# Kernel optimization log

Hardware: AMD Instinct MI355X
Metric: run time of the kernel (lower is better)

## Reference

```python
import jax, jax.numpy as jnp
import numpy as np

N, S, D, H, E, ETYPES = 1024, 64, 256, 4, 4096, 4
HD = D // H
EPS = 1e-5


def setup_inputs() -> dict:
    key = jax.random.key(0)
    ks = jax.random.split(key, 8)
    node_features = jax.random.normal(ks[0], (N, S, D), dtype=jnp.float32)
    lengths = jax.random.randint(ks[1], (N,), 1, S + 1)
    node_masks = (jnp.arange(S)[None, :] < lengths[:, None]).astype(jnp.float32)
    # unique edges (torch builds an adjacency matrix, so duplicates collapse)
    rng = np.random.default_rng(0)
    cand = rng.integers(0, N, size=(4 * E, 2))
    uniq = np.unique(cand, axis=0)
    assert uniq.shape[0] >= E
    perm = rng.permutation(uniq.shape[0])[:E]
    edge_index = jnp.asarray(uniq[perm].T, dtype=jnp.int64)  # [2, E]
    edge_type = jnp.asarray(rng.integers(1, ETYPES + 1, size=(E,)), dtype=jnp.int64)
    scale = 0.02
    wq = jax.random.normal(ks[2], (D, D), jnp.float32) * scale
    wk = jax.random.normal(ks[3], (D, D), jnp.float32) * scale
    wv = jax.random.normal(ks[4], (D, D), jnp.float32) * scale
    wo = jax.random.normal(ks[5], (D, D), jnp.float32) * scale
    return dict(
        node_features=node_features, node_masks=node_masks,
        ln_w=jnp.ones((D,), jnp.float32), ln_b=jnp.zeros((D,), jnp.float32),
        wq=wq, bq=jnp.zeros((D,), jnp.float32),
        wk=wk, bk=jnp.zeros((D,), jnp.float32),
        wv=wv, bv=jnp.zeros((D,), jnp.float32),
        wo=wo, bo=jnp.zeros((D,), jnp.float32),
        edge_type_weights=jnp.ones((ETYPES,), jnp.float32),
        edge_index=edge_index, edge_type=edge_type,
    )


def reference(node_features, node_masks, ln_w, ln_b, wq, bq, wk, bk, wv, bv,
              wo, bo, edge_type_weights, edge_index, edge_type):
    n, s, d = node_features.shape
    # LayerNorm (biased variance, eps=1e-5, as torch)
    mu = jnp.mean(node_features, axis=-1, keepdims=True)
    var = jnp.mean((node_features - mu) ** 2, axis=-1, keepdims=True)
    xn = (node_features - mu) * jax.lax.rsqrt(var + EPS) * ln_w + ln_b
    q = (xn @ wq + bq).reshape(n, s, H, HD)
    k = (xn @ wk + bk).reshape(n, s, H, HD)
    v = (xn @ wv + bv).reshape(n, s, H, HD)
    src, dst = edge_index[0], edge_index[1]
    # per-edge scalar bias: softplus(edge_type_weights[type-1]).clamp(1e-6, 1e6)
    ew = jnp.clip(jax.nn.softplus(edge_type_weights[edge_type - 1]), 1e-6, 1e6)  # [E]
    qe, ke, ve = q[src], k[dst], v[dst]              # [E,S,H,HD]
    km = node_masks[dst]                              # [E,S] key-side mask
    qm = node_masks[src]                              # [E,S] query-side mask
    scores = jnp.einsum('eqhd,ekhd->ehqk', qe, ke) / jnp.sqrt(jnp.float32(HD))
    scores = scores + ew[:, None, None, None]
    neg = jnp.float32(-1e30)
    scores = jnp.where(km[:, None, None, :] > 0, scores, neg)
    # per-edge softmax over the key node's valid tokens; zero rows where no valid key
    attn = jax.nn.softmax(scores, axis=-1) * km[:, None, None, :]
    ctx = jnp.einsum('ehqk,ekhd->eqhd', attn, ve) * qm[:, :, None, None]  # [E,S,H,HD]
    out = jax.ops.segment_sum(ctx, src, num_segments=n)   # sum over incident edges
    out = out.reshape(n, s, d)
    out = out @ wo + bo                                   # output projection (dropout=eval noop)
    out = out + node_features                             # residual
    return out * node_masks[..., None]
```

## Files before the change

kernel.cpp:

```cpp
#include <hip/hip_runtime.h>

#define DDIM 256
#define NEDGE 4096
#define SLEN 64
#define NNODE 1024
#define ROWS 65536

typedef short s16x8 __attribute__((ext_vector_type(8)));
typedef float f32x4 __attribute__((ext_vector_type(4)));

static __device__ __forceinline__ unsigned short f2bf(float f){
  union { float f; unsigned u; } v; v.f = f;
  unsigned r = v.u + 0x7FFFu + ((v.u >> 16) & 1u);
  return (unsigned short)(r >> 16);
}

static __device__ __forceinline__ void gl2lds16(const unsigned short* g, unsigned short* l){
  __builtin_amdgcn_global_load_lds((const __attribute__((address_space(1))) unsigned int*)g,
                                   (__attribute__((address_space(3))) unsigned int*)l, 16, 0, 0);
}

__global__ __launch_bounds__(256) void setup_kernel(const float* nf, const float* lnw, const float* lnb,
                                                    const float* wq, const float* wk, const float* wv, const float* wo,
                                                    const float* bq, const float* bk, const float* bv,
                                                    const float* masks, const int* eidx,
                                                    unsigned short* xn, unsigned short* Wqkv, unsigned short* Wo_t,
                                                    float* qkvb, int* lenp, int* deg){
  int bid = blockIdx.x, tid = threadIdx.x;
  if (bid < 16384){
    int lane = tid & 63;
    int row = bid*4 + (tid >> 6);
    const float4 x4 = ((const float4*)(nf + (size_t)row*DDIM))[lane];
    float s  = x4.x + x4.y + x4.z + x4.w;
    float sq = x4.x*x4.x + x4.y*x4.y + x4.z*x4.z + x4.w*x4.w;
    for (int off=1; off<64; off<<=1){ s += __shfl_xor(s, off); sq += __shfl_xor(sq, off); }
    float mu  = s  * (1.0f/DDIM);
    float var = sq * (1.0f/DDIM) - mu*mu;
    float rs  = rsqrtf(var + 1e-5f);
    float4 w4 = ((const float4*)lnw)[lane];
    float4 b4 = ((const float4*)lnb)[lane];
    ushort4 o;
    o.x = f2bf((x4.x - mu)*rs*w4.x + b4.x);
    o.y = f2bf((x4.y - mu)*rs*w4.y + b4.y);
    o.z = f2bf((x4.z - mu)*rs*w4.z + b4.z);
    o.w = f2bf((x4.w - mu)*rs*w4.w + b4.w);
    ((ushort4*)(xn + (size_t)row*DDIM))[lane] = o;
  } else if (bid < 17412){
    int idx = (bid - 16384)*256 + tid;
    if (idx < 196608){
      int mat = idx >> 16;
      int rem = idx & 65535;
      int n = rem >> 8, k = rem & 255;
      const float* W = (mat==0)?wq:(mat==1)?wk:wv;
      Wqkv[(size_t)(mat*256 + n)*256 + k] = f2bf(W[k*256 + n]);
    } else if (idx < 262144){
      int rem = idx - 196608;
      int n = rem >> 8, k = rem & 255;
      Wo_t[(size_t)n*256 + k] = f2bf(wo[k*256 + n]);
    } else if (idx < 262912){
      int i = idx - 262144;
      qkvb[i] = (i < 256) ? bq[i] : (i < 512) ? bk[i-256] : bv[i-512];
    }
  } else if (bid < 17668){
    int lane = tid & 63;
    int node = (bid - 17412)*4 + (tid >> 6);
    unsigned long long b = __ballot(masks[node*SLEN + lane] > 0.f);
    if (lane == 0) lenp[node] = __popcll(b);
  } else {
    int e = (bid - 17668)*256 + tid;
    if (e < NEDGE) atomicAdd(&deg[eidx[e]], 1);
  }
}

__global__ void scan_kernel(const int* deg, int* startp, int* order){
  __shared__ int buf[NNODE];
  __shared__ int hist[65];
  int t = threadIdx.x;
  int d = deg[t];
  buf[t] = d;
  if (t < 65) hist[t] = 0;
  __syncthreads();
  for (int off=1; off<NNODE; off<<=1){
    int v = (t >= off) ? buf[t-off] : 0;
    __syncthreads();
    buf[t] += v;
    __syncthreads();
  }
  startp[t] = buf[t] - d;
  int dc = d > 64 ? 64 : d;
  atomicAdd(&hist[dc], 1);
  __syncthreads();
  if (t == 0){
    int acc = 0;
    for (int i = 64; i >= 0; i--){ int h = hist[i]; hist[i] = acc; acc += h; }
  }
  __syncthreads();
  int pos = atomicAdd(&hist[dc], 1);
  order[pos] = t;
}

__global__ __launch_bounds__(256) void edge_fill_kernel(const int* eidx, const int* startp, int* cursor, int* elist){
  int e = blockIdx.x*256 + threadIdx.x;
  if (e < NEDGE){
    int s = eidx[e];
    int p = atomicAdd(&cursor[s], 1);
    elist[startp[s] + p] = eidx[NEDGE + e];
  }
}

__global__ __launch_bounds__(256) void qkv_kernel(const unsigned short* xn, const unsigned short* Wqkv,
                                                  const float* qkvb,
                                                  unsigned short* qb, unsigned short* kb_, unsigned short* vb){
  __shared__ __align__(16) unsigned short As[4096];
  __shared__ __align__(16) unsigned short Bs[8192];
  int tid = threadIdx.x;
  int lane = tid & 63, wid = tid >> 6, m = lane & 15, quad = lane >> 4;
  int row0 = blockIdx.x * 64;
  int col0 = blockIdx.y * 128;
  int rw = (wid & 1) * 32, cw = (wid >> 1) * 64;
  f32x4 acc[8];
  #pragma unroll
  for (int i=0;i<8;i++) acc[i] = (f32x4){0.f,0.f,0.f,0.f};
  for (int kc = 0; kc < 4; kc++){
    __syncthreads();
    #pragma unroll
    for (int i=0;i<2;i++){
      int cid = i*256 + tid, row = cid >> 3, c8 = cid & 7;
      gl2lds16(xn + (size_t)(row0 + row)*DDIM + kc*64 + ((c8 ^ (row&7))<<3), As + cid*8);
    }
    #pragma unroll
    for (int i=0;i<4;i++){
      int cid = i*256 + tid, row = cid >> 3, c8 = cid & 7;
      gl2lds16(Wqkv + (size_t)(col0 + row)*DDIM + kc*64 + ((c8 ^ (row&7))<<3), Bs + cid*8);
    }
    __syncthreads();
    #pragma unroll
    for (int ks=0; ks<2; ks++){
      int sw = ((ks*4 + quad) ^ (m&7)) << 3;
      s16x8 af[2], bf[4];
      #pragma unroll
      for (int mt=0;mt<2;mt++) af[mt] = *(const s16x8*)(As + (rw + mt*16 + m)*64 + sw);
      #pragma unroll
      for (int nt=0;nt<4;nt++) bf[nt] = *(const s16x8*)(Bs + (cw + nt*16 + m)*64 + sw);
      #pragma unroll
      for (int mt=0;mt<2;mt++)
        #pragma unroll
        for (int nt=0;nt<4;nt++)
          acc[mt*4+nt] = __builtin_amdgcn_mfma_f32_16x16x32_bf16(af[mt], bf[nt], acc[mt*4+nt], 0,0,0);
    }
  }
  #pragma unroll
  for (int nt=0;nt<4;nt++){
    int cg = col0 + cw + nt*16 + m;
    int mat = cg >> 8, col = cg & 255;
    unsigned short* ob = (mat==0)?qb:(mat==1)?kb_:vb;
    float bb = qkvb[cg];
    #pragma unroll
    for (int mt=0;mt<2;mt++)
      #pragma unroll
      for (int r=0;r<4;r++){
        int row = row0 + rw + mt*16 + quad*4 + r;
        ob[(size_t)row*DDIM + col] = f2bf(acc[mt*4+nt][r] + bb);
      }
  }
}

__global__ __launch_bounds__(256) void attn_kernel(const unsigned short* qb, const unsigned short* kbuf,
                                                   const unsigned short* vb, const int* lenp,
                                                   const int* startp, const int* degp, const int* elist,
                                                   const int* order, unsigned short* ctxb){
  __shared__ __align__(16) unsigned short Kt[2][4096];
  __shared__ unsigned short Vt[2][4096];
  __shared__ unsigned short P[4096];
  int tid = threadIdx.x;
  int lane = tid & 63, wid = tid >> 6, m = lane & 15, quad = lane >> 4;
  int src = order[blockIdx.x], h = blockIdx.y;
  int ls = lenp[src];
  int qtm = (ls + 15) >> 4;
  int s0 = startp[src], dg = degp[src];
  bool active = wid < qtm;
  unsigned short* Pw = P + wid*1024;

  s16x8 qf0 = {0,0,0,0,0,0,0,0}, qf1 = {0,0,0,0,0,0,0,0};
  if (active){
    const unsigned short* qbase = qb + (size_t)(src*SLEN + wid*16 + m)*DDIM + h*64 + quad*8;
    qf0 = *(const s16x8*)(qbase);
    qf1 = *(const s16x8*)(qbase + 32);
  }
  f32x4 o[4];
  #pragma unroll
  for (int i=0;i<4;i++) o[i] = (f32x4){0.f,0.f,0.f,0.f};

  int dstc = 0, ldc = 0;
  if (dg > 0){
    dstc = elist[s0]; ldc = lenp[dstc];
    #pragma unroll
    for (int i=0;i<2;i++){
      int cid = i*256 + tid, row = cid >> 3, c8 = cid & 7;
      gl2lds16(kbuf + (size_t)(dstc*SLEN + row)*DDIM + h*64 + ((c8 ^ (row&7))<<3), Kt[0] + cid*8);
    }
    const unsigned short* vrow = vb + (size_t)(dstc*SLEN + lane)*DDIM + h*64 + wid*16;
    s16x8 v0 = *(const s16x8*)(vrow);
    s16x8 v1 = *(const s16x8*)(vrow + 8);
    #pragma unroll
    for (int j=0;j<8;j++){
      int d = wid*16 + j;
      Vt[0][d*64 + (((lane>>3)^(d&7))<<3) + (lane&7)] = (unsigned short)v0[j];
    }
    #pragma unroll
    for (int j=0;j<8;j++){
      int d = wid*16 + 8 + j;
      Vt[0][d*64 + (((lane>>3)^(d&7))<<3) + (lane&7)] = (unsigned short)v1[j];
    }
  }
  __syncthreads();

  for (int ei=0; ei<dg; ei++){
    int cur = ei & 1, nxt = cur ^ 1;
    bool have_next = (ei+1 < dg);
    int dstn = 0, ldn = 0;
    s16x8 v0n = {0,0,0,0,0,0,0,0}, v1n = {0,0,0,0,0,0,0,0};
    if (have_next){
      dstn = elist[s0 + ei + 1]; ldn = lenp[dstn];
      #pragma unroll
      for (int i=0;i<2;i++){
        int cid = i*256 + tid, row = cid >> 3, c8 = cid & 7;
        gl2lds16(kbuf + (size_t)(dstn*SLEN + row)*DDIM + h*64 + ((c8 ^ (row&7))<<3), Kt[nxt] + cid*8);
      }
      const unsigned short* vrow = vb + (size_t)(dstn*SLEN + lane)*DDIM + h*64 + wid*16;
      v0n = *(const s16x8*)(vrow);
      v1n = *(const s16x8*)(vrow + 8);
    }
    int ktm = (ldc + 15) >> 4;
    int ks2 = (ktm + 1) >> 1;
    if (active){
      f32x4 acc[4];
      #pragma unroll
      for (int i=0;i<4;i++) acc[i] = (f32x4){0.f,0.f,0.f,0.f};
      #pragma unroll
      for (int kt=0; kt<4; kt++) if (kt < ktm){
        int key = kt*16 + m;
        s16x8 b0 = *(const s16x8*)(Kt[cur] + key*64 + ((quad ^ (m&7))<<3));
        acc[kt] = __builtin_amdgcn_mfma_f32_16x16x32_bf16(qf0, b0, acc[kt], 0,0,0);
        s16x8 b1 = *(const s16x8*)(Kt[cur] + key*64 + (((4 + quad) ^ (m&7))<<3));
        acc[kt] = __builtin_amdgcn_mfma_f32_16x16x32_bf16(qf1, b1, acc[kt], 0,0,0);
      }
      #pragma unroll
      for (int r=0; r<4; r++){
        float x[4];
        #pragma unroll
        for (int kt=0; kt<4; kt++)
          x[kt] = (kt < ktm && kt*16 + m < ldc) ? __expf(acc[kt][r]*0.125f) : 0.f;
        float s = x[0] + x[1] + x[2] + x[3];
        for (int off=1; off<16; off<<=1) s += __shfl_xor(s, off);
        float inv = 1.0f / s;
        int q = quad*4 + r;
        #pragma unroll
        for (int kt=0; kt<4; kt++) if (kt < 2*ks2){
          int key = kt*16 + m;
          Pw[q*64 + (((key>>3)^(q&7))<<3) + (key&7)] = f2bf(x[kt]*inv);
        }
      }
      #pragma unroll
      for (int ks=0; ks<2; ks++) if (ks < ks2){
        s16x8 pa = *(const s16x8*)(Pw + m*64 + ((((ks*4+quad))^(m&7))<<3));
        #pragma unroll
        for (int dt=0; dt<4; dt++){
          int d = dt*16 + m;
          s16x8 vf = *(const s16x8*)(Vt[cur] + d*64 + (((ks*4+quad)^(d&7))<<3));
          o[dt] = __builtin_amdgcn_mfma_f32_16x16x32_bf16(pa, vf, o[dt], 0,0,0);
        }
      }
    }
    if (have_next){
      #pragma unroll
      for (int j=0;j<8;j++){
        int d = wid*16 + j;
        Vt[nxt][d*64 + (((lane>>3)^(d&7))<<3) + (lane&7)] = (unsigned short)v0n[j];
      }
      #pragma unroll
      for (int j=0;j<8;j++){
        int d = wid*16 + 8 + j;
        Vt[nxt][d*64 + (((lane>>3)^(d&7))<<3) + (lane&7)] = (unsigned short)v1n[j];
      }
      dstc = dstn; ldc = ldn;
    }
    __syncthreads();
  }
  if (active){
    #pragma unroll
    for (int dt=0; dt<4; dt++){
      int col = h*64 + dt*16 + m;
      #pragma unroll
      for (int r=0; r<4; r++){
        int row = src*SLEN + wid*16 + quad*4 + r;
        ctxb[(size_t)row*DDIM + col] = f2bf(o[dt][r]);
      }
    }
  }
}

__global__ __launch_bounds__(256) void out_kernel(const unsigned short* ctxb, const unsigned short* Wo_t,
                                                  const float* bo, const float* nf, const float* masks,
                                                  float* out){
  __shared__ __align__(16) unsigned short As[4096];
  __shared__ __align__(16) unsigned short Bs[8192];
  int tid = threadIdx.x;
  int lane = tid & 63, wid = tid >> 6, m = lane & 15, quad = lane >> 4;
  int row0 = blockIdx.x * 64;
  int col0 = blockIdx.y * 128;
  int rw = (wid & 1) * 32, cw = (wid >> 1) * 64;
  f32x4 acc[8];
  #pragma unroll
  for (int i=0;i<8;i++) acc[i] = (f32x4){0.f,0.f,0.f,0.f};
  for (int kc = 0; kc < 4; kc++){
    __syncthreads();
    #pragma unroll
    for (int i=0;i<2;i++){
      int cid = i*256 + tid, row = cid >> 3, c8 = cid & 7;
      gl2lds16(ctxb + (size_t)(row0 + row)*DDIM + kc*64 + ((c8 ^ (row&7))<<3), As + cid*8);
    }
    #pragma unroll
    for (int i=0;i<4;i++){
      int cid = i*256 + tid, row = cid >> 3, c8 = cid & 7;
      gl2lds16(Wo_t + (size_t)(col0 + row)*DDIM + kc*64 + ((c8 ^ (row&7))<<3), Bs + cid*8);
    }
    __syncthreads();
    #pragma unroll
    for (int ks=0; ks<2; ks++){
      int sw = ((ks*4 + quad) ^ (m&7)) << 3;
      s16x8 af[2], bf[4];
      #pragma unroll
      for (int mt=0;mt<2;mt++) af[mt] = *(const s16x8*)(As + (rw + mt*16 + m)*64 + sw);
      #pragma unroll
      for (int nt=0;nt<4;nt++) bf[nt] = *(const s16x8*)(Bs + (cw + nt*16 + m)*64 + sw);
      #pragma unroll
      for (int mt=0;mt<2;mt++)
        #pragma unroll
        for (int nt=0;nt<4;nt++)
          acc[mt*4+nt] = __builtin_amdgcn_mfma_f32_16x16x32_bf16(af[mt], bf[nt], acc[mt*4+nt], 0,0,0);
    }
  }
  #pragma unroll
  for (int nt=0;nt<4;nt++){
    int col = col0 + cw + nt*16 + m;
    float bb = bo[col];
    #pragma unroll
    for (int mt=0;mt<2;mt++)
      #pragma unroll
      for (int r=0;r<4;r++){
        int row = row0 + rw + mt*16 + quad*4 + r;
        float v = acc[mt*4+nt][r] + bb + nf[(size_t)row*DDIM + col];
        out[(size_t)row*DDIM + col] = v * masks[row];
      }
  }
}

extern "C" void kernel_launch(void* const* d_in, const int* in_sizes, int n_in,
                              void* d_out, int out_size, void* d_ws, size_t ws_size,
                              hipStream_t stream){
  const float* nf    = (const float*)d_in[0];
  const float* masks = (const float*)d_in[1];
  const float* lnw   = (const float*)d_in[2];
  const float* lnb   = (const float*)d_in[3];
  const float* wq    = (const float*)d_in[4];
  const float* bq    = (const float*)d_in[5];
  const float* wk    = (const float*)d_in[6];
  const float* bk    = (const float*)d_in[7];
  const float* wv    = (const float*)d_in[8];
  const float* bv    = (const float*)d_in[9];
  const float* wo    = (const float*)d_in[10];
  const float* bo    = (const float*)d_in[11];
  const int*   eidx  = (const int*)d_in[13];
  float* out = (float*)d_out;

  char* ws = (char*)d_ws;
  const size_t B = (size_t)ROWS * DDIM * 2;
  unsigned short* xn   = (unsigned short*)(ws);
  unsigned short* qb   = (unsigned short*)(ws + B);
  unsigned short* kb   = (unsigned short*)(ws + 2*B);
  unsigned short* vb   = (unsigned short*)(ws + 3*B);
  unsigned short* ctxb = (unsigned short*)(ws + 4*B);
  char* wp = ws + 5*B;
  unsigned short* Wqkv = (unsigned short*)(wp);
  unsigned short* Wo_t = (unsigned short*)(wp + 393216);
  float* qkvb         = (float*)(wp + 524288);
  char* ip = wp + 528384;
  int* deg    = (int*)(ip);
  int* cursor = (int*)(ip + 4096);
  int* startp = (int*)(ip + 8192);
  int* lenp   = (int*)(ip + 12288);
  int* order  = (int*)(ip + 16384);
  int* elist  = (int*)(ip + 20480);

  hipMemsetAsync(deg, 0, 8192, stream);
  setup_kernel<<<17684, 256, 0, stream>>>(nf, lnw, lnb, wq, wk, wv, wo, bq, bk, bv,
                                          masks, eidx, xn, Wqkv, Wo_t, qkvb, lenp, deg);
  scan_kernel<<<1, NNODE, 0, stream>>>(deg, startp, order);
  edge_fill_kernel<<<NEDGE/256, 256, 0, stream>>>(eidx, startp, cursor, elist);
  qkv_kernel<<<dim3(ROWS/64, 6), 256, 0, stream>>>(xn, Wqkv, qkvb, qb, kb, vb);
  attn_kernel<<<dim3(NNODE, 4), 256, 0, stream>>>(qb, kb, vb, lenp, startp, deg, elist, order, ctxb);
  out_kernel<<<dim3(ROWS/64, 2), 256, 0, stream>>>(ctxb, Wo_t, bo, nf, masks, out);
}
```

Measured before the change: 348.5 us.

## Store V transposed per node and stream K/V into LDS asynchronously

The QKV GEMM now writes V in a per-node, per-feature transposed layout (node, dim, token), so the attention kernel can load V tiles with async global-to-LDS copies. This replaces the register load plus scattered transpose stores into LDS. K loads now skip 16-row chunks past the destination's valid length, and the next destination index is prefetched one edge further ahead. The cost is strided 8-byte V stores in the GEMM epilogue, and LDS tails of K beyond the valid length are left stale, which is safe only because those keys are masked.

```diff
diff --git a/kernel.cpp b/kernel.cpp
--- a/kernel.cpp
+++ b/kernel.cpp
@@ -110,7 +110,7 @@
 
 __global__ __launch_bounds__(256) void qkv_kernel(const unsigned short* xn, const unsigned short* Wqkv,
                                                   const float* qkvb,
-                                                  unsigned short* qb, unsigned short* kb_, unsigned short* vb){
+                                                  unsigned short* qb, unsigned short* kb_, unsigned short* vt){
   __shared__ __align__(16) unsigned short As[4096];
   __shared__ __align__(16) unsigned short Bs[8192];
   int tid = threadIdx.x;
@@ -149,28 +149,42 @@
           acc[mt*4+nt] = __builtin_amdgcn_mfma_f32_16x16x32_bf16(af[mt], bf[nt], acc[mt*4+nt], 0,0,0);
     }
   }
+  int node = row0 >> 6;
   #pragma unroll
   for (int nt=0;nt<4;nt++){
     int cg = col0 + cw + nt*16 + m;
     int mat = cg >> 8, col = cg & 255;
-    unsigned short* ob = (mat==0)?qb:(mat==1)?kb_:vb;
     float bb = qkvb[cg];
-    #pragma unroll
-    for (int mt=0;mt<2;mt++)
-      #pragma unroll
-      for (int r=0;r<4;r++){
-        int row = row0 + rw + mt*16 + quad*4 + r;
-        ob[(size_t)row*DDIM + col] = f2bf(acc[mt*4+nt][r] + bb);
-      }
+    if (mat < 2){
+      unsigned short* ob = (mat==0)?qb:kb_;
+      #pragma unroll
+      for (int mt=0;mt<2;mt++)
+        #pragma unroll
+        for (int r=0;r<4;r++){
+          int row = row0 + rw + mt*16 + quad*4 + r;
+          ob[(size_t)row*DDIM + col] = f2bf(acc[mt*4+nt][r] + bb);
+        }
+    } else {
+      #pragma unroll
+      for (int mt=0;mt<2;mt++){
+        int tok0 = rw + mt*16 + quad*4;
+        ushort4 p;
+        p.x = f2bf(acc[mt*4+nt][0] + bb);
+        p.y = f2bf(acc[mt*4+nt][1] + bb);
+        p.z = f2bf(acc[mt*4+nt][2] + bb);
+        p.w = f2bf(acc[mt*4+nt][3] + bb);
+        *(ushort4*)(vt + ((size_t)node*256 + col)*64 + tok0) = p;
+      }
+    }
   }
 }
 
 __global__ __launch_bounds__(256) void attn_kernel(const unsigned short* qb, const unsigned short* kbuf,
-                                                   const unsigned short* vb, const int* lenp,
+                                                   const unsigned short* vtb, const int* lenp,
                                                    const int* startp, const int* degp, const int* elist,
                                                    const int* order, unsigned short* ctxb){
   __shared__ __align__(16) unsigned short Kt[2][4096];
-  __shared__ unsigned short Vt[2][4096];
+  __shared__ __align__(16) unsigned short Vt[2][4096];
   __shared__ unsigned short P[4096];
   int tid = threadIdx.x;
   int lane = tid & 63, wid = tid >> 6, m = lane & 15, quad = lane >> 4;
@@ -191,47 +205,52 @@
   #pragma unroll
   for (int i=0;i<4;i++) o[i] = (f32x4){0.f,0.f,0.f,0.f};
 
-  int dstc = 0, ldc = 0;
+  int dst0 = 0, dst1 = 0, ld0 = 0;
   if (dg > 0){
-    dstc = elist[s0]; ldc = lenp[dstc];
+    dst0 = elist[s0];
+    ld0 = lenp[dst0];
+    int kch = ((ld0 + 15) >> 4) * 128;
+    #pragma unroll
+    for (int i=0;i<2;i++){
+      int cid = i*256 + tid;
+      if (i*256 + wid*64 < kch){
+        int row = cid >> 3, c8 = cid & 7;
+        gl2lds16(kbuf + (size_t)(dst0*SLEN + row)*DDIM + h*64 + ((c8 ^ (row&7))<<3), Kt[0] + cid*8);
+      }
+    }
+    const unsigned short* vhead = vtb + ((size_t)dst0*256 + h*64)*64;
     #pragma unroll
     for (int i=0;i<2;i++){
       int cid = i*256 + tid, row = cid >> 3, c8 = cid & 7;
-      gl2lds16(kbuf + (size_t)(dstc*SLEN + row)*DDIM + h*64 + ((c8 ^ (row&7))<<3), Kt[0] + cid*8);
-    }
-    const unsigned short* vrow = vb + (size_t)(dstc*SLEN + lane)*DDIM + h*64 + wid*16;
-    s16x8 v0 = *(const s16x8*)(vrow);
-    s16x8 v1 = *(const s16x8*)(vrow + 8);
-    #pragma unroll
-    for (int j=0;j<8;j++){
-      int d = wid*16 + j;
-      Vt[0][d*64 + (((lane>>3)^(d&7))<<3) + (lane&7)] = (unsigned short)v0[j];
-    }
-    #pragma unroll
-    for (int j=0;j<8;j++){
-      int d = wid*16 + 8 + j;
-      Vt[0][d*64 + (((lane>>3)^(d&7))<<3) + (lane&7)] = (unsigned short)v1[j];
-    }
-  }
+      gl2lds16(vhead + row*64 + ((c8 ^ (row&7))<<3), Vt[0] + cid*8);
+    }
+  }
+  if (dg > 1) dst1 = elist[s0 + 1];
   __syncthreads();
 
   for (int ei=0; ei<dg; ei++){
     int cur = ei & 1, nxt = cur ^ 1;
-    bool have_next = (ei+1 < dg);
-    int dstn = 0, ldn = 0;
-    s16x8 v0n = {0,0,0,0,0,0,0,0}, v1n = {0,0,0,0,0,0,0,0};
-    if (have_next){
-      dstn = elist[s0 + ei + 1]; ldn = lenp[dstn];
+    int dst2 = (ei+2 < dg) ? elist[s0 + ei + 2] : 0;
+    int ld1 = 0;
+    if (ei+1 < dg){
+      ld1 = lenp[dst1];
+      int kch = ((ld1 + 15) >> 4) * 128;
+      #pragma unroll
+      for (int i=0;i<2;i++){
+        int cid = i*256 + tid;
+        if (i*256 + wid*64 < kch){
+          int row = cid >> 3, c8 = cid & 7;
+          gl2lds16(kbuf + (size_t)(dst1*SLEN + row)*DDIM + h*64 + ((c8 ^ (row&7))<<3), Kt[nxt] + cid*8);
+        }
+      }
+      const unsigned short* vhead = vtb + ((size_t)dst1*256 + h*64)*64;
       #pragma unroll
       for (int i=0;i<2;i++){
         int cid = i*256 + tid, row = cid >> 3, c8 = cid & 7;
-        gl2lds16(kbuf + (size_t)(dstn*SLEN + row)*DDIM + h*64 + ((c8 ^ (row&7))<<3), Kt[nxt] + cid*8);
-      }
-      const unsigned short* vrow = vb + (size_t)(dstn*SLEN + lane)*DDIM + h*64 + wid*16;
-      v0n = *(const s16x8*)(vrow);
-      v1n = *(const s16x8*)(vrow + 8);
-    }
-    int ktm = (ldc + 15) >> 4;
+        gl2lds16(vhead + row*64 + ((c8 ^ (row&7))<<3), Vt[nxt] + cid*8);
+      }
+    }
+    int ktm = (ld0 + 15) >> 4;
     int ks2 = (ktm + 1) >> 1;
     if (active){
       f32x4 acc[4];
@@ -250,7 +269,7 @@
         float x[4];
         #pragma unroll
         for (int kt=0; kt<4; kt++)
-          x[kt] = (kt < ktm && kt*16 + m < ldc) ? __expf(acc[kt][r]*0.125f) : 0.f;
+          x[kt] = (kt < ktm && kt*16 + m < ld0) ? __expf(acc[kt][r]*0.125f) : 0.f;
         float s = x[0] + x[1] + x[2] + x[3];
         for (int off=1; off<16; off<<=1) s += __shfl_xor(s, off);
         float inv = 1.0f / s;
@@ -272,19 +291,7 @@
         }
       }
     }
-    if (have_next){
-      #pragma unroll
-      for (int j=0;j<8;j++){
-        int d = wid*16 + j;
-        Vt[nxt][d*64 + (((lane>>3)^(d&7))<<3) + (lane&7)] = (unsigned short)v0n[j];
-      }
-      #pragma unroll
-      for (int j=0;j<8;j++){
-        int d = wid*16 + 8 + j;
-        Vt[nxt][d*64 + (((lane>>3)^(d&7))<<3) + (lane&7)] = (unsigned short)v1n[j];
-      }
-      dstc = dstn; ldc = ldn;
-    }
+    dst0 = dst1; ld0 = ld1; dst1 = dst2;
     __syncthreads();
   }
   if (active){
@@ -379,7 +386,7 @@
   unsigned short* xn   = (unsigned short*)(ws);
   unsigned short* qb   = (unsigned short*)(ws + B);
   unsigned short* kb   = (unsigned short*)(ws + 2*B);
-  unsigned short* vb   = (unsigned short*)(ws + 3*B);
+  unsigned short* vt   = (unsigned short*)(ws + 3*B);
   unsigned short* ctxb = (unsigned short*)(ws + 4*B);
   char* wp = ws + 5*B;
   unsigned short* Wqkv = (unsigned short*)(wp);
@@ -398,7 +405,7 @@
                                           masks, eidx, xn, Wqkv, Wo_t, qkvb, lenp, deg);
   scan_kernel<<<1, NNODE, 0, stream>>>(deg, startp, order);
   edge_fill_kernel<<<NEDGE/256, 256, 0, stream>>>(eidx, startp, cursor, elist);
-  qkv_kernel<<<dim3(ROWS/64, 6), 256, 0, stream>>>(xn, Wqkv, qkvb, qb, kb, vb);
-  attn_kernel<<<dim3(NNODE, 4), 256, 0, stream>>>(qb, kb, vb, lenp, startp, deg, elist, order, ctxb);
+  qkv_kernel<<<dim3(ROWS/64, 6), 256, 0, stream>>>(xn, Wqkv, qkvb, qb, kb, vt);
+  attn_kernel<<<dim3(NNODE, 4), 256, 0, stream>>>(qb, kb, vt, lenp, startp, deg, elist, order, ctxb);
   out_kernel<<<dim3(ROWS/64, 2), 256, 0, stream>>>(ctxb, Wo_t, bo, nf, masks, out);
 }
```

After: 352.0 us. About the same (+1.0%).
